# Performance work log

Hardware: AMD Instinct MI355X
Metric: run time of the kernel (lower is better)

## Reference

```python
import jax, jax.numpy as jnp
import numpy as np

MARGIN = 1.0
N, D = 8192, 128
NUM_CLASSES = 43


def setup_inputs() -> dict:
    key = jax.random.key(0)
    kx, ky = jax.random.split(key)
    x = jax.random.normal(kx, (N, D), dtype=jnp.float32)
    y = jax.random.randint(ky, (N,), 0, NUM_CLASSES, dtype=jnp.int64)
    return {"x": x, "y": y}


def reference(x, y):
    # Pairwise squared distances between rows of x: [N, N].
    # Equivalent to the original tile/permute construction, but via GEMM:
    # ||a-b||^2 = ||a||^2 + ||b||^2 - 2 a.b
    sq = jnp.sum(x * x, axis=1)                      # [N]
    norms = sq[:, None] + sq[None, :] - 2.0 * (x @ x.T)  # [N, N]
    maxims = jnp.maximum(MARGIN - norms, 0.0)        # [N, N]

    # Same-label mask (1 where labels equal, 0 otherwise).
    equalities = (y[:, None] == y[None, :]).astype(norms.dtype)  # [N, N]
    eye = jnp.eye(x.shape[0], dtype=norms.dtype)

    pos_mask = equalities - eye       # positive pairs, excluding self
    neg_mask = 1.0 - equalities       # negative pairs

    pos_term = jnp.sum(pos_mask * norms) / jnp.sum(pos_mask)
    neg_term = jnp.sum(neg_mask * maxims) / jnp.sum(neg_mask)
    return (pos_term + neg_term) / 2.0
```

## Files before the change

kernel.cpp:

```cpp
#include <hip/hip_runtime.h>

#define N_ROWS 8192
#define DIM 128
#define NCLS 43
#define TILE 256
#define TILES2 32
#define NPAIRS2 528
#define NBLOCKS 256

typedef __attribute__((ext_vector_type(8))) __bf16 bf16x8;
typedef __attribute__((ext_vector_type(4))) float float4v;
typedef __attribute__((address_space(1))) const void global_cvoid;
typedef __attribute__((address_space(3))) void lds_void;

#define SM_B    65536
#define SM_SQY  131072
#define SM_RED  139264
#define SM_FLAG 139456
#define SM_SIZE 139520

__device__ __forceinline__ unsigned short f2bf(float f) {
    unsigned int u = __float_as_uint(f);
    u += 0x7FFFu + ((u >> 16) & 1u);
    return (unsigned short)(u >> 16);
}

__device__ __forceinline__ void decode_tile(int t, int& bi, int& bj) {
    int b = (int)((65.0f - sqrtf((float)(65 * 65 - 8 * t))) * 0.5f);
    if (b < 0) b = 0;
    if (b > TILES2 - 1) b = TILES2 - 1;
    while (b * TILES2 - (b * (b - 1)) / 2 > t) --b;
    while ((b + 1) * TILES2 - ((b + 1) * b) / 2 <= t) ++b;
    bi = b; bj = b + (t - (b * TILES2 - (b * (b - 1)) / 2));
}

__device__ __forceinline__ void stage_tile(
        const unsigned short* xbf, const float* sq, const int* y,
        char* smem, int bi, int bj, int par, int wv, int lane) {
    const char* srcA = (const char*)(xbf + (size_t)bi * TILE * DIM);
    const char* srcB = (const char*)(xbf + (size_t)bj * TILE * DIM);
    #pragma unroll
    for (int it = 0; it < 4; ++it) {
        int pbase = (it * 16 + wv) * 1024;
        int p = pbase + lane * 16;
        int r = p >> 8;
        int c = ((p >> 4) & 15) ^ (r & 15);
        int goff = (r << 8) + (c << 4);
        __builtin_amdgcn_global_load_lds(
            (global_cvoid*)(srcA + goff), (lds_void*)(smem + pbase), 16, 0, 0);
        __builtin_amdgcn_global_load_lds(
            (global_cvoid*)(srcB + goff), (lds_void*)(smem + SM_B + pbase), 16, 0, 0);
    }
    if (wv < 4) {
        const char* src = (wv == 0) ? (const char*)(sq + bi * TILE)
                        : (wv == 1) ? (const char*)(sq + bj * TILE)
                        : (wv == 2) ? (const char*)(y  + bi * TILE)
                                    : (const char*)(y  + bj * TILE);
        __builtin_amdgcn_global_load_lds(
            (global_cvoid*)(src + lane * 16),
            (lds_void*)(smem + SM_SQY + par * 4096 + wv * 1024), 16, 0, 0);
    }
}

__global__ void __launch_bounds__(256) prep_kernel(
        const float* __restrict__ x,
        float* __restrict__ sq,
        unsigned short* __restrict__ xbf,
        int* __restrict__ counter) {
    if (blockIdx.x == 0 && threadIdx.x == 0) *counter = 0;
    int wave = threadIdx.x >> 6;
    int lane = threadIdx.x & 63;
    int half = lane >> 5, l32 = lane & 31;
    int row  = blockIdx.x * 8 + wave * 2 + half;
    const float4 v = *(const float4*)(x + (size_t)row * DIM + l32 * 4);
    ushort4 b; b.x = f2bf(v.x); b.y = f2bf(v.y); b.z = f2bf(v.z); b.w = f2bf(v.w);
    *(ushort4*)(xbf + (size_t)row * DIM + l32 * 4) = b;
    float s = v.x * v.x + v.y * v.y + v.z * v.z + v.w * v.w;
    #pragma unroll
    for (int off = 16; off > 0; off >>= 1) s += __shfl_down(s, off);
    if (l32 == 0) sq[row] = s;
}

__global__ void __launch_bounds__(1024, 4) tile_kernel(
        const unsigned short* __restrict__ xbf,
        const float* __restrict__ sq,
        const int* __restrict__ y,
        float2* __restrict__ partials,
        int* __restrict__ counter,
        float* __restrict__ out) {
    __shared__ __align__(16) char smem[SM_SIZE];

    int b    = blockIdx.x;
    int wv   = threadIdx.x >> 6;
    int lane = threadIdx.x & 63;
    int m    = lane & 15;
    int quad = lane >> 4;
    int wr   = (wv >> 2) * 64;
    int wc   = (wv & 3) * 64;
    int ibase = wr + quad * 4;
    int jbase = wc + m;

    float posAcc = 0.f, negAcc = 0.f;
    int parity = 0;

    {
        int bi, bj; decode_tile(b, bi, bj);
        stage_tile(xbf, sq, y, smem, bi, bj, 0, wv, lane);
    }
    __syncthreads();

    for (int t = b; t < NPAIRS2; t += NBLOCKS) {
        int bi, bj; decode_tile(t, bi, bj);

        float4v acc[4][4];
        #pragma unroll
        for (int a = 0; a < 4; ++a)
            #pragma unroll
            for (int c = 0; c < 4; ++c) {
                float4v z = {0.f, 0.f, 0.f, 0.f};
                acc[a][c] = z;
            }

        #pragma unroll
        for (int ks = 0; ks < 4; ++ks) {
            int chunk = ((ks * 4 + quad) ^ m) * 16;
            bf16x8 af[4], bfr[4];
            #pragma unroll
            for (int ti = 0; ti < 4; ++ti)
                af[ti] = *(const bf16x8*)(smem + (wr + ti * 16 + m) * 256 + chunk);
            #pragma unroll
            for (int tj = 0; tj < 4; ++tj)
                bfr[tj] = *(const bf16x8*)(smem + SM_B + (wc + tj * 16 + m) * 256 + chunk);
            #pragma unroll
            for (int ti = 0; ti < 4; ++ti)
                #pragma unroll
                for (int tj = 0; tj < 4; ++tj)
                    acc[ti][tj] = __builtin_amdgcn_mfma_f32_16x16x32_bf16(
                                      af[ti], bfr[tj], acc[ti][tj], 0, 0, 0);
        }
        __syncthreads();

        int tn = t + NBLOCKS;
        if (tn < NPAIRS2) {
            int nbi, nbj; decode_tile(tn, nbi, nbj);
            stage_tile(xbf, sq, y, smem, nbi, nbj, parity ^ 1, wv, lane);
        }

        const float* sqA = (const float*)(smem + SM_SQY + parity * 4096);
        const float* sqB = sqA + 256;
        const int*   yA  = (const int*)(sqA + 512);
        const int*   yB  = (const int*)(sqA + 768);

        float sqj[4]; int yj[4];
        #pragma unroll
        for (int tj = 0; tj < 4; ++tj) {
            sqj[tj] = sqB[jbase + tj * 16];
            yj[tj]  = yB [jbase + tj * 16];
        }
        float sqjmin = fminf(fminf(sqj[0], sqj[1]), fminf(sqj[2], sqj[3]));
        float posD = 0.f, dotmax = -3e38f, sqimin = 3e38f;

        if (bi != bj) {
            #pragma unroll
            for (int ti = 0; ti < 4; ++ti) {
                #pragma unroll
                for (int r = 0; r < 4; ++r) {
                    int il = ibase + ti * 16 + r;
                    float sqi = sqA[il]; int yi = yA[il];
                    sqimin = fminf(sqimin, sqi);
                    #pragma unroll
                    for (int tj = 0; tj < 4; ++tj) {
                        float d = acc[ti][tj][r];
                        posD += (yi == yj[tj]) ? d : 0.f;
                        dotmax = fmaxf(dotmax, d);
                    }
                }
            }
        } else {
            #pragma unroll
            for (int ti = 0; ti < 4; ++ti) {
                #pragma unroll
                for (int r = 0; r < 4; ++r) {
                    int il = ibase + ti * 16 + r;
                    float sqi = sqA[il]; int yi = yA[il];
                    sqimin = fminf(sqimin, sqi);
                    #pragma unroll
                    for (int tj = 0; tj < 4; ++tj) {
                        int jl = jbase + tj * 16;
                        bool self = (il == jl);
                        float d = acc[ti][tj][r];
                        posD += (yi == yj[tj] && !self) ? d : 0.f;
                        dotmax = fmaxf(dotmax, self ? -3e38f : d);
                    }
                }
            }
        }

        float negS = 0.f;
        if (2.f * dotmax - sqimin - sqjmin >= -1.f) {
            #pragma unroll
            for (int ti = 0; ti < 4; ++ti)
                #pragma unroll
                for (int r = 0; r < 4; ++r) {
                    int il = ibase + ti * 16 + r;
                    float sqi = sqA[il]; int yi = yA[il];
                    #pragma unroll
                    for (int tj = 0; tj < 4; ++tj)
                        if (yi != yj[tj]) {
                            float nrm = fmaf(-2.f, acc[ti][tj][r], sqi + sqj[tj]);
                            negS += fmaxf(1.f - nrm, 0.f);
                        }
                }
        }
        float wgt = (bi == bj) ? 1.f : 2.f;
        posAcc += wgt * posD;
        negAcc += wgt * negS;

        parity ^= 1;
        __syncthreads();
    }

    #pragma unroll
    for (int off = 32; off > 0; off >>= 1) {
        posAcc += __shfl_down(posAcc, off);
        negAcc += __shfl_down(negAcc, off);
    }
    float2* pred  = (float2*)(smem + SM_RED);
    float*  swred = (float*)(smem + SM_RED + 128);
    int*    flag  = (int*)(smem + SM_FLAG);
    if (lane == 0) pred[wv] = make_float2(posAcc, negAcc);
    __syncthreads();
    if (threadIdx.x == 0) {
        float ps = 0.f, ns = 0.f;
        #pragma unroll
        for (int w = 0; w < 16; ++w) { ps += pred[w].x; ns += pred[w].y; }
        partials[b] = make_float2(ps, ns);
        __threadfence();
        int old = atomicAdd(counter, 1);
        *flag = (old == NBLOCKS - 1) ? 1 : 0;
    }
    __syncthreads();
    if (*flag == 0) return;

    __threadfence();
    int tid = threadIdx.x;
    int* hists = (int*)smem;
    int* htot  = (int*)smem + 16 * 48;
    for (int i = tid; i < 16 * 48 + 48; i += 1024) ((int*)smem)[i] = 0;
    __syncthreads();

    const int4* y4 = (const int4*)y;
    int4 ya = y4[tid], yb = y4[tid + 1024];
    atomicAdd(&hists[wv * 48 + ya.x], 1); atomicAdd(&hists[wv * 48 + ya.y], 1);
    atomicAdd(&hists[wv * 48 + ya.z], 1); atomicAdd(&hists[wv * 48 + ya.w], 1);
    atomicAdd(&hists[wv * 48 + yb.x], 1); atomicAdd(&hists[wv * 48 + yb.y], 1);
    atomicAdd(&hists[wv * 48 + yb.z], 1); atomicAdd(&hists[wv * 48 + yb.w], 1);
    __syncthreads();
    if (tid < 48) {
        int nc = 0;
        #pragma unroll
        for (int w = 0; w < 16; ++w) nc += hists[w * 48 + tid];
        htot[tid] = nc;
    }
    __syncthreads();

    const float4* sq4 = (const float4*)sq;
    float4 sa = sq4[tid], sb = sq4[tid + 1024];
    float sw = sa.x * (float)(htot[ya.x] - 1) + sa.y * (float)(htot[ya.y] - 1)
             + sa.z * (float)(htot[ya.z] - 1) + sa.w * (float)(htot[ya.w] - 1)
             + sb.x * (float)(htot[yb.x] - 1) + sb.y * (float)(htot[yb.y] - 1)
             + sb.z * (float)(htot[yb.z] - 1) + sb.w * (float)(htot[yb.w] - 1);

    float p = 0.f, n = 0.f;
    if (tid < NBLOCKS) { float2 v = partials[tid]; p = v.x; n = v.y; }
    #pragma unroll
    for (int off = 32; off > 0; off >>= 1) {
        sw += __shfl_down(sw, off);
        p  += __shfl_down(p, off);
        n  += __shfl_down(n, off);
    }
    if (lane == 0) { pred[wv] = make_float2(p, n); swred[wv] = sw; }
    __syncthreads();
    if (tid == 0) {
        float PS = 0.f, NS = 0.f, SW = 0.f;
        #pragma unroll
        for (int w = 0; w < 16; ++w) { PS += pred[w].x; NS += pred[w].y; SW += swred[w]; }
        long long s2 = 0;
        for (int c = 0; c < NCLS; ++c) { long long h = htot[c]; s2 += h * h; }
        float posc = (float)(s2 - (long long)N_ROWS);
        float negc = (float)((long long)N_ROWS * N_ROWS - s2);
        out[0] = 0.5f * ((2.f * SW - 2.f * PS) / posc + NS / negc);
    }
}

extern "C" void kernel_launch(void* const* d_in, const int* in_sizes, int n_in,
                              void* d_out, int out_size, void* d_ws, size_t ws_size,
                              hipStream_t stream) {
    const float* x = (const float*)d_in[0];
    const int*   y = (const int*)d_in[1];
    float* out = (float*)d_out;

    char* ws = (char*)d_ws;
    float2*         partials = (float2*)ws;
    int*            counter  = (int*)(ws + 2048);
    float*          sq       = (float*)(ws + 2560);
    unsigned short* xbf      = (unsigned short*)(ws + 35328);

    prep_kernel<<<N_ROWS / 8, 256, 0, stream>>>(x, sq, xbf, counter);
    tile_kernel<<<NBLOCKS, 1024, 0, stream>>>(xbf, sq, y, partials, counter, out);
}
```

Baseline: 88.41 us.

## Use 128-row tiles with one block per tile pair and separate finish kernel

Replaces the persistent 256-block, 1024-thread kernel, which double-buffers 256x256 tile pairs, with a grid of 2080 blocks of 256 threads. Each block computes a single 128x128 upper-triangular tile pair. The last-block atomic counter reduction becomes a separate single-block finish kernel. The goal is better occupancy and load balance: each block uses less LDS and there are many more blocks to fill the CUs. The cost is losing the cross-tile prefetch overlap, an extra kernel launch, and more redundant loading of tile data.

```diff
diff --git a/kernel.cpp b/kernel.cpp
--- a/kernel.cpp
+++ b/kernel.cpp
@@ -3,21 +3,22 @@
 #define N_ROWS 8192
 #define DIM 128
 #define NCLS 43
-#define TILE 256
-#define TILES2 32
-#define NPAIRS2 528
-#define NBLOCKS 256
+#define TILE 128
+#define TILES 64
+#define NPAIRS 2080
 
 typedef __attribute__((ext_vector_type(8))) __bf16 bf16x8;
 typedef __attribute__((ext_vector_type(4))) float float4v;
 typedef __attribute__((address_space(1))) const void global_cvoid;
 typedef __attribute__((address_space(3))) void lds_void;
 
-#define SM_B    65536
-#define SM_SQY  131072
-#define SM_RED  139264
-#define SM_FLAG 139456
-#define SM_SIZE 139520
+#define SM_B   32768
+#define SM_SQA 65536
+#define SM_SQB 66048
+#define SM_YA  66560
+#define SM_YB  67072
+#define SM_RED 67584
+#define SM_SIZE 67648
 
 __device__ __forceinline__ unsigned short f2bf(float f) {
     unsigned int u = __float_as_uint(f);
@@ -25,23 +26,46 @@
     return (unsigned short)(u >> 16);
 }
 
-__device__ __forceinline__ void decode_tile(int t, int& bi, int& bj) {
-    int b = (int)((65.0f - sqrtf((float)(65 * 65 - 8 * t))) * 0.5f);
-    if (b < 0) b = 0;
-    if (b > TILES2 - 1) b = TILES2 - 1;
-    while (b * TILES2 - (b * (b - 1)) / 2 > t) --b;
-    while ((b + 1) * TILES2 - ((b + 1) * b) / 2 <= t) ++b;
-    bi = b; bj = b + (t - (b * TILES2 - (b * (b - 1)) / 2));
-}
-
-__device__ __forceinline__ void stage_tile(
-        const unsigned short* xbf, const float* sq, const int* y,
-        char* smem, int bi, int bj, int par, int wv, int lane) {
+__global__ void __launch_bounds__(256) prep_kernel(
+        const float* __restrict__ x,
+        float* __restrict__ sq,
+        unsigned short* __restrict__ xbf) {
+    int wave = threadIdx.x >> 6;
+    int lane = threadIdx.x & 63;
+    int half = lane >> 5, l32 = lane & 31;
+    int row  = blockIdx.x * 8 + wave * 2 + half;
+    const float4 v = *(const float4*)(x + (size_t)row * DIM + l32 * 4);
+    ushort4 b; b.x = f2bf(v.x); b.y = f2bf(v.y); b.z = f2bf(v.z); b.w = f2bf(v.w);
+    *(ushort4*)(xbf + (size_t)row * DIM + l32 * 4) = b;
+    float s = v.x * v.x + v.y * v.y + v.z * v.z + v.w * v.w;
+    #pragma unroll
+    for (int off = 16; off > 0; off >>= 1) s += __shfl_down(s, off);
+    if (l32 == 0) sq[row] = s;
+}
+
+__global__ void __launch_bounds__(256) tile_kernel(
+        const unsigned short* __restrict__ xbf,
+        const float* __restrict__ sq,
+        const int* __restrict__ y,
+        float2* __restrict__ partials) {
+    __shared__ __align__(16) char smem[SM_SIZE];
+
+    int t = blockIdx.x;
+    int bi = (int)((129.0f - sqrtf((float)(129 * 129 - 8 * t))) * 0.5f);
+    if (bi < 0) bi = 0;
+    if (bi > TILES - 1) bi = TILES - 1;
+    while (bi * TILES - (bi * (bi - 1)) / 2 > t) --bi;
+    while ((bi + 1) * TILES - ((bi + 1) * bi) / 2 <= t) ++bi;
+    int bj = bi + (t - (bi * TILES - (bi * (bi - 1)) / 2));
+
+    int wv   = threadIdx.x >> 6;
+    int lane = threadIdx.x & 63;
+
     const char* srcA = (const char*)(xbf + (size_t)bi * TILE * DIM);
     const char* srcB = (const char*)(xbf + (size_t)bj * TILE * DIM);
     #pragma unroll
-    for (int it = 0; it < 4; ++it) {
-        int pbase = (it * 16 + wv) * 1024;
+    for (int it = 0; it < 8; ++it) {
+        int pbase = (it * 4 + wv) * 1024;
         int p = pbase + lane * 16;
         int r = p >> 8;
         int c = ((p >> 4) & 15) ^ (r & 15);
@@ -51,215 +75,159 @@
         __builtin_amdgcn_global_load_lds(
             (global_cvoid*)(srcB + goff), (lds_void*)(smem + SM_B + pbase), 16, 0, 0);
     }
-    if (wv < 4) {
-        const char* src = (wv == 0) ? (const char*)(sq + bi * TILE)
-                        : (wv == 1) ? (const char*)(sq + bj * TILE)
-                        : (wv == 2) ? (const char*)(y  + bi * TILE)
-                                    : (const char*)(y  + bj * TILE);
-        __builtin_amdgcn_global_load_lds(
-            (global_cvoid*)(src + lane * 16),
-            (lds_void*)(smem + SM_SQY + par * 4096 + wv * 1024), 16, 0, 0);
-    }
-}
-
-__global__ void __launch_bounds__(256) prep_kernel(
-        const float* __restrict__ x,
-        float* __restrict__ sq,
-        unsigned short* __restrict__ xbf,
-        int* __restrict__ counter) {
-    if (blockIdx.x == 0 && threadIdx.x == 0) *counter = 0;
-    int wave = threadIdx.x >> 6;
-    int lane = threadIdx.x & 63;
-    int half = lane >> 5, l32 = lane & 31;
-    int row  = blockIdx.x * 8 + wave * 2 + half;
-    const float4 v = *(const float4*)(x + (size_t)row * DIM + l32 * 4);
-    ushort4 b; b.x = f2bf(v.x); b.y = f2bf(v.y); b.z = f2bf(v.z); b.w = f2bf(v.w);
-    *(ushort4*)(xbf + (size_t)row * DIM + l32 * 4) = b;
-    float s = v.x * v.x + v.y * v.y + v.z * v.z + v.w * v.w;
-    #pragma unroll
-    for (int off = 16; off > 0; off >>= 1) s += __shfl_down(s, off);
-    if (l32 == 0) sq[row] = s;
-}
-
-__global__ void __launch_bounds__(1024, 4) tile_kernel(
-        const unsigned short* __restrict__ xbf,
-        const float* __restrict__ sq,
-        const int* __restrict__ y,
-        float2* __restrict__ partials,
-        int* __restrict__ counter,
-        float* __restrict__ out) {
-    __shared__ __align__(16) char smem[SM_SIZE];
-
-    int b    = blockIdx.x;
-    int wv   = threadIdx.x >> 6;
-    int lane = threadIdx.x & 63;
+    {
+        int ti = threadIdx.x;
+        if (ti < 128)  ((float*)(smem + SM_SQA))[ti]       = sq[bi * TILE + ti];
+        else           ((float*)(smem + SM_SQB))[ti - 128] = sq[bj * TILE + ti - 128];
+        if (ti < 128)  ((int*)  (smem + SM_YA ))[ti]       = y [bi * TILE + ti];
+        else           ((int*)  (smem + SM_YB ))[ti - 128] = y [bj * TILE + ti - 128];
+    }
+    __syncthreads();
+
     int m    = lane & 15;
     int quad = lane >> 4;
-    int wr   = (wv >> 2) * 64;
-    int wc   = (wv & 3) * 64;
+    int wr   = (wv >> 1) * 64;
+    int wc   = (wv & 1) * 64;
+
+    float4v acc[4][4];
+    #pragma unroll
+    for (int a = 0; a < 4; ++a)
+        #pragma unroll
+        for (int c = 0; c < 4; ++c) {
+            float4v z = {0.f, 0.f, 0.f, 0.f};
+            acc[a][c] = z;
+        }
+
+    #pragma unroll
+    for (int ks = 0; ks < 4; ++ks) {
+        int chunk = ((ks * 4 + quad) ^ m) * 16;
+        bf16x8 af[4], bfr[4];
+        #pragma unroll
+        for (int ti = 0; ti < 4; ++ti)
+            af[ti] = *(const bf16x8*)(smem + (wr + ti * 16 + m) * 256 + chunk);
+        #pragma unroll
+        for (int tj = 0; tj < 4; ++tj)
+            bfr[tj] = *(const bf16x8*)(smem + SM_B + (wc + tj * 16 + m) * 256 + chunk);
+        #pragma unroll
+        for (int ti = 0; ti < 4; ++ti)
+            #pragma unroll
+            for (int tj = 0; tj < 4; ++tj)
+                acc[ti][tj] = __builtin_amdgcn_mfma_f32_16x16x32_bf16(
+                                  af[ti], bfr[tj], acc[ti][tj], 0, 0, 0);
+    }
+
+    const float* sqA = (const float*)(smem + SM_SQA);
+    const float* sqB = (const float*)(smem + SM_SQB);
+    const int*   yA  = (const int*)  (smem + SM_YA);
+    const int*   yB  = (const int*)  (smem + SM_YB);
     int ibase = wr + quad * 4;
     int jbase = wc + m;
 
-    float posAcc = 0.f, negAcc = 0.f;
-    int parity = 0;
-
-    {
-        int bi, bj; decode_tile(b, bi, bj);
-        stage_tile(xbf, sq, y, smem, bi, bj, 0, wv, lane);
-    }
-    __syncthreads();
-
-    for (int t = b; t < NPAIRS2; t += NBLOCKS) {
-        int bi, bj; decode_tile(t, bi, bj);
-
-        float4v acc[4][4];
-        #pragma unroll
-        for (int a = 0; a < 4; ++a)
-            #pragma unroll
-            for (int c = 0; c < 4; ++c) {
-                float4v z = {0.f, 0.f, 0.f, 0.f};
-                acc[a][c] = z;
-            }
-
-        #pragma unroll
-        for (int ks = 0; ks < 4; ++ks) {
-            int chunk = ((ks * 4 + quad) ^ m) * 16;
-            bf16x8 af[4], bfr[4];
-            #pragma unroll
-            for (int ti = 0; ti < 4; ++ti)
-                af[ti] = *(const bf16x8*)(smem + (wr + ti * 16 + m) * 256 + chunk);
-            #pragma unroll
-            for (int tj = 0; tj < 4; ++tj)
-                bfr[tj] = *(const bf16x8*)(smem + SM_B + (wc + tj * 16 + m) * 256 + chunk);
-            #pragma unroll
-            for (int ti = 0; ti < 4; ++ti)
+    float sqj[4]; int yj[4];
+    #pragma unroll
+    for (int tj = 0; tj < 4; ++tj) {
+        sqj[tj] = sqB[jbase + tj * 16];
+        yj[tj]  = yB [jbase + tj * 16];
+    }
+    float sqjmin = fminf(fminf(sqj[0], sqj[1]), fminf(sqj[2], sqj[3]));
+    float posD = 0.f, dotmax = -3e38f, sqimin = 3e38f;
+
+    if (bi != bj) {
+        #pragma unroll
+        for (int ti = 0; ti < 4; ++ti) {
+            #pragma unroll
+            for (int r = 0; r < 4; ++r) {
+                int il = ibase + ti * 16 + r;
+                float sqi = sqA[il]; int yi = yA[il];
+                sqimin = fminf(sqimin, sqi);
                 #pragma unroll
-                for (int tj = 0; tj < 4; ++tj)
-                    acc[ti][tj] = __builtin_amdgcn_mfma_f32_16x16x32_bf16(
-                                      af[ti], bfr[tj], acc[ti][tj], 0, 0, 0);
-        }
-        __syncthreads();
-
-        int tn = t + NBLOCKS;
-        if (tn < NPAIRS2) {
-            int nbi, nbj; decode_tile(tn, nbi, nbj);
-            stage_tile(xbf, sq, y, smem, nbi, nbj, parity ^ 1, wv, lane);
-        }
-
-        const float* sqA = (const float*)(smem + SM_SQY + parity * 4096);
-        const float* sqB = sqA + 256;
-        const int*   yA  = (const int*)(sqA + 512);
-        const int*   yB  = (const int*)(sqA + 768);
-
-        float sqj[4]; int yj[4];
-        #pragma unroll
-        for (int tj = 0; tj < 4; ++tj) {
-            sqj[tj] = sqB[jbase + tj * 16];
-            yj[tj]  = yB [jbase + tj * 16];
-        }
-        float sqjmin = fminf(fminf(sqj[0], sqj[1]), fminf(sqj[2], sqj[3]));
-        float posD = 0.f, dotmax = -3e38f, sqimin = 3e38f;
-
-        if (bi != bj) {
-            #pragma unroll
-            for (int ti = 0; ti < 4; ++ti) {
-                #pragma unroll
-                for (int r = 0; r < 4; ++r) {
-                    int il = ibase + ti * 16 + r;
-                    float sqi = sqA[il]; int yi = yA[il];
-                    sqimin = fminf(sqimin, sqi);
-                    #pragma unroll
-                    for (int tj = 0; tj < 4; ++tj) {
-                        float d = acc[ti][tj][r];
-                        posD += (yi == yj[tj]) ? d : 0.f;
-                        dotmax = fmaxf(dotmax, d);
-                    }
-                }
-            }
-        } else {
-            #pragma unroll
-            for (int ti = 0; ti < 4; ++ti) {
-                #pragma unroll
-                for (int r = 0; r < 4; ++r) {
-                    int il = ibase + ti * 16 + r;
-                    float sqi = sqA[il]; int yi = yA[il];
-                    sqimin = fminf(sqimin, sqi);
-                    #pragma unroll
-                    for (int tj = 0; tj < 4; ++tj) {
-                        int jl = jbase + tj * 16;
-                        bool self = (il == jl);
-                        float d = acc[ti][tj][r];
-                        posD += (yi == yj[tj] && !self) ? d : 0.f;
-                        dotmax = fmaxf(dotmax, self ? -3e38f : d);
-                    }
+                for (int tj = 0; tj < 4; ++tj) {
+                    float d = acc[ti][tj][r];
+                    posD += (yi == yj[tj]) ? d : 0.f;
+                    dotmax = fmaxf(dotmax, d);
                 }
             }
         }
-
-        float negS = 0.f;
-        if (2.f * dotmax - sqimin - sqjmin >= -1.f) {
-            #pragma unroll
-            for (int ti = 0; ti < 4; ++ti)
+    } else {
+        #pragma unroll
+        for (int ti = 0; ti < 4; ++ti) {
+            #pragma unroll
+            for (int r = 0; r < 4; ++r) {
+                int il = ibase + ti * 16 + r;
+                float sqi = sqA[il]; int yi = yA[il];
+                sqimin = fminf(sqimin, sqi);
                 #pragma unroll
-                for (int r = 0; r < 4; ++r) {
-                    int il = ibase + ti * 16 + r;
-                    float sqi = sqA[il]; int yi = yA[il];
-                    #pragma unroll
-                    for (int tj = 0; tj < 4; ++tj)
-                        if (yi != yj[tj]) {
-                            float nrm = fmaf(-2.f, acc[ti][tj][r], sqi + sqj[tj]);
-                            negS += fmaxf(1.f - nrm, 0.f);
-                        }
+                for (int tj = 0; tj < 4; ++tj) {
+                    int jl = jbase + tj * 16;
+                    bool self = (il == jl);
+                    float d = acc[ti][tj][r];
+                    posD += (yi == yj[tj] && !self) ? d : 0.f;
+                    dotmax = fmaxf(dotmax, self ? -3e38f : d);
                 }
+            }
         }
-        float wgt = (bi == bj) ? 1.f : 2.f;
-        posAcc += wgt * posD;
-        negAcc += wgt * negS;
-
-        parity ^= 1;
-        __syncthreads();
-    }
+    }
+
+    float negS = 0.f;
+    if (2.f * dotmax - sqimin - sqjmin >= -1.f) {
+        #pragma unroll
+        for (int ti = 0; ti < 4; ++ti)
+            #pragma unroll
+            for (int r = 0; r < 4; ++r) {
+                int il = ibase + ti * 16 + r;
+                float sqi = sqA[il]; int yi = yA[il];
+                #pragma unroll
+                for (int tj = 0; tj < 4; ++tj)
+                    if (yi != yj[tj]) {
+                        float nrm = fmaf(-2.f, acc[ti][tj][r], sqi + sqj[tj]);
+                        negS += fmaxf(1.f - nrm, 0.f);
+                    }
+            }
+    }
+    float wgt = (bi == bj) ? 1.f : 2.f;
+    float posP = wgt * posD;
+    float negP = wgt * negS;
 
     #pragma unroll
     for (int off = 32; off > 0; off >>= 1) {
-        posAcc += __shfl_down(posAcc, off);
-        negAcc += __shfl_down(negAcc, off);
-    }
-    float2* pred  = (float2*)(smem + SM_RED);
-    float*  swred = (float*)(smem + SM_RED + 128);
-    int*    flag  = (int*)(smem + SM_FLAG);
-    if (lane == 0) pred[wv] = make_float2(posAcc, negAcc);
+        posP += __shfl_down(posP, off);
+        negP += __shfl_down(negP, off);
+    }
+    float2* wred = (float2*)(smem + SM_RED);
+    if (lane == 0) wred[wv] = make_float2(posP, negP);
     __syncthreads();
     if (threadIdx.x == 0) {
-        float ps = 0.f, ns = 0.f;
-        #pragma unroll
-        for (int w = 0; w < 16; ++w) { ps += pred[w].x; ns += pred[w].y; }
-        partials[b] = make_float2(ps, ns);
-        __threadfence();
-        int old = atomicAdd(counter, 1);
-        *flag = (old == NBLOCKS - 1) ? 1 : 0;
-    }
-    __syncthreads();
-    if (*flag == 0) return;
-
-    __threadfence();
-    int tid = threadIdx.x;
-    int* hists = (int*)smem;
-    int* htot  = (int*)smem + 16 * 48;
-    for (int i = tid; i < 16 * 48 + 48; i += 1024) ((int*)smem)[i] = 0;
+        float2 a0 = wred[0], a1 = wred[1], a2 = wred[2], a3 = wred[3];
+        partials[t] = make_float2(a0.x + a1.x + a2.x + a3.x,
+                                  a0.y + a1.y + a2.y + a3.y);
+    }
+}
+
+__global__ void __launch_bounds__(1024) finish_kernel(
+        const float2* __restrict__ partials,
+        const int* __restrict__ y,
+        const float* __restrict__ sq,
+        float* __restrict__ out) {
+    __shared__ int hists[16][48];
+    __shared__ int htot[48];
+    __shared__ float2 red[16];
+    __shared__ float swred[16];
+    int tid = threadIdx.x, wv = tid >> 6, lane = tid & 63;
+
+    for (int i = tid; i < 16 * 48; i += 1024) ((int*)hists)[i] = 0;
     __syncthreads();
 
     const int4* y4 = (const int4*)y;
     int4 ya = y4[tid], yb = y4[tid + 1024];
-    atomicAdd(&hists[wv * 48 + ya.x], 1); atomicAdd(&hists[wv * 48 + ya.y], 1);
-    atomicAdd(&hists[wv * 48 + ya.z], 1); atomicAdd(&hists[wv * 48 + ya.w], 1);
-    atomicAdd(&hists[wv * 48 + yb.x], 1); atomicAdd(&hists[wv * 48 + yb.y], 1);
-    atomicAdd(&hists[wv * 48 + yb.z], 1); atomicAdd(&hists[wv * 48 + yb.w], 1);
+    atomicAdd(&hists[wv][ya.x], 1); atomicAdd(&hists[wv][ya.y], 1);
+    atomicAdd(&hists[wv][ya.z], 1); atomicAdd(&hists[wv][ya.w], 1);
+    atomicAdd(&hists[wv][yb.x], 1); atomicAdd(&hists[wv][yb.y], 1);
+    atomicAdd(&hists[wv][yb.z], 1); atomicAdd(&hists[wv][yb.w], 1);
     __syncthreads();
     if (tid < 48) {
         int nc = 0;
         #pragma unroll
-        for (int w = 0; w < 16; ++w) nc += hists[w * 48 + tid];
+        for (int w = 0; w < 16; ++w) nc += hists[w][tid];
         htot[tid] = nc;
     }
     __syncthreads();
@@ -272,19 +240,22 @@
              + sb.z * (float)(htot[yb.z] - 1) + sb.w * (float)(htot[yb.w] - 1);
 
     float p = 0.f, n = 0.f;
-    if (tid < NBLOCKS) { float2 v = partials[tid]; p = v.x; n = v.y; }
+    for (int i = tid; i < NPAIRS; i += 1024) {
+        float2 v = partials[i];
+        p += v.x; n += v.y;
+    }
     #pragma unroll
     for (int off = 32; off > 0; off >>= 1) {
         sw += __shfl_down(sw, off);
         p  += __shfl_down(p, off);
         n  += __shfl_down(n, off);
     }
-    if (lane == 0) { pred[wv] = make_float2(p, n); swred[wv] = sw; }
+    if (lane == 0) { red[wv] = make_float2(p, n); swred[wv] = sw; }
     __syncthreads();
     if (tid == 0) {
         float PS = 0.f, NS = 0.f, SW = 0.f;
         #pragma unroll
-        for (int w = 0; w < 16; ++w) { PS += pred[w].x; NS += pred[w].y; SW += swred[w]; }
+        for (int w = 0; w < 16; ++w) { PS += red[w].x; NS += red[w].y; SW += swred[w]; }
         long long s2 = 0;
         for (int c = 0; c < NCLS; ++c) { long long h = htot[c]; s2 += h * h; }
         float posc = (float)(s2 - (long long)N_ROWS);
@@ -302,10 +273,10 @@
 
     char* ws = (char*)d_ws;
     float2*         partials = (float2*)ws;
-    int*            counter  = (int*)(ws + 2048);
-    float*          sq       = (float*)(ws + 2560);
-    unsigned short* xbf      = (unsigned short*)(ws + 35328);
-
-    prep_kernel<<<N_ROWS / 8, 256, 0, stream>>>(x, sq, xbf, counter);
-    tile_kernel<<<NBLOCKS, 1024, 0, stream>>>(xbf, sq, y, partials, counter, out);
-}
+    float*          sq       = (float*)(ws + 16896);
+    unsigned short* xbf      = (unsigned short*)(ws + 49920);
+
+    prep_kernel<<<N_ROWS / 8, 256, 0, stream>>>(x, sq, xbf);
+    tile_kernel<<<NPAIRS, 256, 0, stream>>>(xbf, sq, y, partials);
+    finish_kernel<<<1, 1024, 0, stream>>>(partials, y, sq, out);
+}
```

Result: faster. 82.58 us (-6.6%).
